# Optimization experiments

Hardware: AMD Instinct MI355X
Metric: run time of the kernel (lower is better)

## Reference

```python
import jax, jax.numpy as jnp
import numpy as np

N_NODES = 100000
N_EDGES = 1600000
D_IN = 128
D_HID = 128
N_CLASSES = 40


def _glorot(key, fan_in, fan_out):
    lim = np.sqrt(6.0 / (fan_in + fan_out)).astype(np.float32)
    return jax.random.uniform(key, (fan_in, fan_out), jnp.float32, -lim, lim)


def setup_inputs() -> dict:
    key = jax.random.key(0)
    ks = jax.random.split(key, 10)
    x = jax.random.normal(ks[0], (N_NODES, D_IN), jnp.float32)
    edge_index = jax.random.randint(ks[1], (2, N_EDGES), 0, N_NODES, jnp.int64)
    return {
        "x": x,
        "edge_index": edge_index,
        # layer 1: lin_l (neighbor, with bias), lin_r (root, no bias)
        "W1l": _glorot(ks[2], D_IN, D_HID),
        "b1": jnp.zeros((D_HID,), jnp.float32),
        "W1r": _glorot(ks[3], D_IN, D_HID),
        # layer 2
        "W2l": _glorot(ks[4], D_HID, D_HID),
        "b2": jnp.zeros((D_HID,), jnp.float32),
        "W2r": _glorot(ks[5], D_HID, D_HID),
        # layer 3
        "W3l": _glorot(ks[6], D_HID, N_CLASSES),
        "b3": jnp.zeros((N_CLASSES,), jnp.float32),
        "W3r": _glorot(ks[7], D_HID, N_CLASSES),
    }


def _sage_conv(x, src, dst, deg_inv, Wl, bl, Wr):
    # mean aggregation of source-node features onto destination nodes
    msgs = x[src]                                            # [E, d] gather
    agg = jax.ops.segment_sum(msgs, dst, num_segments=N_NODES)  # [N, d]
    agg = agg * deg_inv[:, None]                             # mean
    return agg @ Wl + bl + x @ Wr


def reference(x, edge_index, W1l, b1, W1r, W2l, b2, W2r, W3l, b3, W3r):
    src, dst = edge_index[0], edge_index[1]
    deg = jax.ops.segment_sum(jnp.ones((N_EDGES,), x.dtype), dst,
                              num_segments=N_NODES)
    deg_inv = 1.0 / jnp.maximum(deg, 1.0)
    h = _sage_conv(x, src, dst, deg_inv, W1l, b1, W1r)
    h = jax.nn.relu(h)  # dropout is identity in eval mode
    h = _sage_conv(h, src, dst, deg_inv, W2l, b2, W2r)
    h = jax.nn.relu(h)
    h = _sage_conv(h, src, dst, deg_inv, W3l, b3, W3r)
    return jax.nn.log_softmax(h, axis=1)
```

## Files before the change

kernel.cpp:

```cpp
#include <hip/hip_runtime.h>
#include <math.h>

#define D 128
#define NCLS 40
#define NBLK_P1 256

typedef unsigned int u32;
typedef __attribute__((ext_vector_type(8))) short short8;
typedef __attribute__((ext_vector_type(4))) float f32x4;

__device__ inline float bflo(u32 u){ return __uint_as_float(u << 16); }
__device__ inline float bfhi(u32 u){ return __uint_as_float(u & 0xffff0000u); }
__device__ inline u32 pack2bf(float a, float b){
  u32 ua = __float_as_uint(a), ub = __float_as_uint(b);
  ua += 0x7fffu + ((ua >> 16) & 1u);
  ub += 0x7fffu + ((ub >> 16) & 1u);
  return (ua >> 16) | (ub & 0xffff0000u);
}
__device__ inline unsigned short pack1bf(float a){
  u32 ua = __float_as_uint(a);
  ua += 0x7fffu + ((ua >> 16) & 1u);
  return (unsigned short)(ua >> 16);
}

__global__ __launch_bounds__(256) void prep_k(
    const float4* __restrict__ x4, uint2* __restrict__ xb, int n4,
    const float* __restrict__ W1l, const float* __restrict__ W1r, u32* __restrict__ Wt1,
    const float* __restrict__ W2l, const float* __restrict__ W2r, u32* __restrict__ Wt2,
    const float* __restrict__ W3l, const float* __restrict__ W3r,
    u32* __restrict__ Wt3b, float* __restrict__ bias3b, const float* __restrict__ b3,
    const int* __restrict__ dst, int* __restrict__ gcnt, int E, int nbuk, int nbX)
{
  __shared__ int cnt[1024];
  const int b = blockIdx.x;
  const int tid = threadIdx.x;
  if (b < nbX){
    int i = b * 256 + tid;
    if (i < n4){
      float4 v = x4[i];
      xb[i] = make_uint2(pack2bf(v.x, v.y), pack2bf(v.z, v.w));
    }
  } else if (b < nbX + 128){
    const bool first = (b < nbX + 64);
    const float* Wl = first ? W1l : W2l;
    const float* Wr = first ? W1r : W2r;
    u32* Wt = first ? Wt1 : Wt2;
    int i = ((b - nbX) & 63) * 256 + tid;
    int nn = i >> 7, kp = i & 127;
    int k = kp * 2;
    float a, c;
    if (k < 128){ a = Wl[(size_t)k * 128 + nn]; c = Wl[(size_t)(k + 1) * 128 + nn]; }
    else        { a = Wr[(size_t)(k - 128) * 128 + nn]; c = Wr[(size_t)(k - 127) * 128 + nn]; }
    Wt[(size_t)nn * 128 + kp] = pack2bf(a, c);
  } else if (b < nbX + 160){
    int i = (b - nbX - 128) * 256 + tid;
    if (i < 128 * 64){
      int nn = i >> 6, kp = i & 63;
      int k = kp * 2;
      float a = 0.f, c = 0.f;
      if (nn < NCLS){
        a = W3l[(size_t)k * NCLS + nn]; c = W3l[(size_t)(k + 1) * NCLS + nn];
      } else if (nn >= 64 && nn < 64 + NCLS){
        int cc = nn - 64;
        a = W3r[(size_t)k * NCLS + cc]; c = W3r[(size_t)(k + 1) * NCLS + cc];
      }
      Wt3b[(size_t)nn * 64 + kp] = pack2bf(a, c);
    }
    if (b == nbX + 128 && tid < 128)
      bias3b[tid] = (tid >= 64 && tid < 64 + NCLS) ? b3[tid - 64] : 0.f;
  } else {
    const int hb = b - nbX - 160;
    for (int i = tid; i < nbuk; i += 256) cnt[i] = 0;
    __syncthreads();
    const int per = (E + NBLK_P1 - 1) / NBLK_P1;
    const int e0 = hb * per;
    const int e1 = min(e0 + per, E);
    for (int i = e0 + tid; i < e1; i += 256)
      atomicAdd(&cnt[dst[i] >> 7], 1);
    __syncthreads();
    for (int i = tid; i < nbuk; i += 256)
      gcnt[(size_t)hb * nbuk + i] = cnt[i];
  }
}


__global__ __launch_bounds__(256) void bsum_k(
    const int* __restrict__ gcnt, int* __restrict__ btot, int nbuk)
{
  __shared__ int sm[256];
  const int j = blockIdx.x;
  sm[threadIdx.x] = gcnt[(size_t)threadIdx.x * nbuk + j];
  __syncthreads();
  for (int off = 128; off > 0; off >>= 1){
    if (threadIdx.x < off) sm[threadIdx.x] += sm[threadIdx.x + off];
    __syncthreads();
  }
  if (threadIdx.x == 0) btot[j] = sm[0];
}

__global__ __launch_bounds__(1024) void scan_k(
    const int* __restrict__ btot, int* __restrict__ bbase, int nbuk)
{
  __shared__ int sm[1024];
  const int j = threadIdx.x;
  int v = (j < nbuk) ? btot[j] : 0;
  sm[j] = v;
  __syncthreads();
  int acc = v;
  for (int off = 1; off < 1024; off <<= 1){
    int t = (j >= off) ? sm[j - off] : 0;
    __syncthreads();
    acc += t; sm[j] = acc;
    __syncthreads();
  }
  if (j < nbuk){
    bbase[j] = acc - v;
    if (j == nbuk - 1) bbase[nbuk] = acc;
  }
}

__global__ __launch_bounds__(256) void goff_k(
    const int* __restrict__ gcnt, const int* __restrict__ bbase,
    int* __restrict__ goff, int nbuk)
{
  __shared__ int sm[256];
  const int j = blockIdx.x;
  const int i = threadIdx.x;
  int v = gcnt[(size_t)i * nbuk + j];
  sm[i] = v;
  __syncthreads();
  int acc = v;
  for (int off = 1; off < 256; off <<= 1){
    int t = (i >= off) ? sm[i - off] : 0;
    __syncthreads();
    acc += t; sm[i] = acc;
    __syncthreads();
  }
  goff[(size_t)i * nbuk + j] = bbase[j] + acc - v;
}

__global__ __launch_bounds__(256) void part_fill_k(
    const int* __restrict__ src, const int* __restrict__ dst,
    const int* __restrict__ goff, u32* __restrict__ staging,
    int E, int nbuk)
{
  __shared__ int boff[1024];
  __shared__ int cur[1024];
  const int tid = threadIdx.x;
  for (int i = tid; i < nbuk; i += 256){
    boff[i] = goff[(size_t)blockIdx.x * nbuk + i];
    cur[i] = 0;
  }
  __syncthreads();
  const int per = (E + NBLK_P1 - 1) / NBLK_P1;
  const int e0 = blockIdx.x * per;
  const int e1 = min(e0 + per, E);
  for (int i = e0 + tid; i < e1; i += 256){
    int d = dst[i];
    int s = src[i];
    int b = d >> 7;
    int p = atomicAdd(&cur[b], 1);
    staging[boff[b] + p] = ((u32)s << 7) | (u32)(d & 127);
  }
}

__global__ __launch_bounds__(256) void bucket_csr_k(
    const u32* __restrict__ staging, const int* __restrict__ bbase,
    int* __restrict__ csr_off, float* __restrict__ deg_inv,
    int* __restrict__ csr_src, int N)
{
  __shared__ int ldeg[128];
  __shared__ int sm[128];
  __shared__ int lbase[128];
  __shared__ int lpos[128];
  const int b = blockIdx.x;
  const int node0 = b << 7;
  const int tid = threadIdx.x;
  if (tid < 128) ldeg[tid] = 0;
  __syncthreads();
  const int lo = bbase[b], hi = bbase[b + 1];
  for (int i = lo + tid; i < hi; i += 256)
    atomicAdd(&ldeg[staging[i] & 127u], 1);
  __syncthreads();
  if (tid < 128) sm[tid] = ldeg[tid];
  __syncthreads();
  for (int off = 1; off < 128; off <<= 1){
    int t = (tid >= off && tid < 128) ? sm[tid - off] : 0;
    __syncthreads();
    if (tid < 128) sm[tid] += t;
    __syncthreads();
  }
  if (tid < 128){
    const int excl = sm[tid] - ldeg[tid];
    lbase[tid] = lo + excl;
    lpos[tid] = 0;
    const int node = node0 + tid;
    if (node < N){
      csr_off[node] = lo + excl;
      deg_inv[node] = 1.0f / fmaxf((float)ldeg[tid], 1.0f);
    } else if (node == N){
      csr_off[N] = lo + excl;
    }
  }
  if (tid == 0 && b == (int)gridDim.x - 1) csr_off[N] = hi;
  __syncthreads();
  for (int i = lo + tid; i < hi; i += 256){
    u32 v = staging[i];
    int dloc = (int)(v & 127u);
    int p = atomicAdd(&lpos[dloc], 1);
    csr_src[lbase[dloc] + p] = (int)(v >> 7);
  }
}

__device__ inline void add8(float* acc, uint4 v){
  acc[0] += bflo(v.x); acc[1] += bfhi(v.x);
  acc[2] += bflo(v.y); acc[3] += bfhi(v.y);
  acc[4] += bflo(v.z); acc[5] += bfhi(v.z);
  acc[6] += bflo(v.w); acc[7] += bfhi(v.w);
}

__global__ __launch_bounds__(256) void aggregate_k(
    const u32* __restrict__ feat, const int* __restrict__ coff,
    const int* __restrict__ csr_src, const float* __restrict__ deg_inv,
    u32* __restrict__ agg, int n)
{
  const int g = threadIdx.x >> 4;
  const int lane = threadIdx.x & 15;
  const int node = blockIdx.x * 16 + g;
  if (node >= n) return;
  const int lo = coff[node], hi = coff[node + 1];
  const uint4* __restrict__ f4 = (const uint4*)feat;
  float acc[8] = {0.f,0.f,0.f,0.f,0.f,0.f,0.f,0.f};
  int e = lo;
  for (; e + 7 < hi; e += 8){
    int s0 = csr_src[e],     s1 = csr_src[e + 1];
    int s2 = csr_src[e + 2], s3 = csr_src[e + 3];
    int s4 = csr_src[e + 4], s5 = csr_src[e + 5];
    int s6 = csr_src[e + 6], s7 = csr_src[e + 7];
    uint4 v0 = f4[(size_t)s0 * 16 + lane];
    uint4 v1 = f4[(size_t)s1 * 16 + lane];
    uint4 v2 = f4[(size_t)s2 * 16 + lane];
    uint4 v3 = f4[(size_t)s3 * 16 + lane];
    uint4 v4 = f4[(size_t)s4 * 16 + lane];
    uint4 v5 = f4[(size_t)s5 * 16 + lane];
    uint4 v6 = f4[(size_t)s6 * 16 + lane];
    uint4 v7 = f4[(size_t)s7 * 16 + lane];
    add8(acc, v0); add8(acc, v1); add8(acc, v2); add8(acc, v3);
    add8(acc, v4); add8(acc, v5); add8(acc, v6); add8(acc, v7);
  }
  for (; e + 3 < hi; e += 4){
    int s0 = csr_src[e],     s1 = csr_src[e + 1];
    int s2 = csr_src[e + 2], s3 = csr_src[e + 3];
    uint4 v0 = f4[(size_t)s0 * 16 + lane];
    uint4 v1 = f4[(size_t)s1 * 16 + lane];
    uint4 v2 = f4[(size_t)s2 * 16 + lane];
    uint4 v3 = f4[(size_t)s3 * 16 + lane];
    add8(acc, v0); add8(acc, v1); add8(acc, v2); add8(acc, v3);
  }
  for (; e < hi; ++e){
    uint4 v0 = f4[(size_t)csr_src[e] * 16 + lane];
    add8(acc, v0);
  }
  const float di = deg_inv[node];
  uint4 o;
  o.x = pack2bf(acc[0] * di, acc[1] * di);
  o.y = pack2bf(acc[2] * di, acc[3] * di);
  o.z = pack2bf(acc[4] * di, acc[5] * di);
  o.w = pack2bf(acc[6] * di, acc[7] * di);
  ((uint4*)agg)[(size_t)node * 16 + lane] = o;
}

__global__ __launch_bounds__(256) void gemm_mfma_k(
    const u32* __restrict__ A1, const u32* __restrict__ A2,
    const u32* __restrict__ Wt, const float* __restrict__ bias,
    u32* __restrict__ out, int n)
{
  __shared__ u32 smem[8704];
  u32* As_u = smem;
  u32* Bs_u = smem + 2560;
  const int tid = threadIdx.x;
  const int row0 = blockIdx.x * 128;
  const int l = tid & 63, w = tid >> 6;
  const int lm = l & 15, lq = l >> 4;

  f32x4 acc[2][8];
  #pragma unroll
  for (int mi = 0; mi < 2; mi++)
    #pragma unroll
    for (int ni = 0; ni < 8; ni++) acc[mi][ni] = (f32x4){0.f, 0.f, 0.f, 0.f};

  for (int kt = 0; kt < 8; ++kt){
    const u32* Ap = (kt < 4) ? A1 : A2;
    const int ko = (kt & 3) * 16;
    #pragma unroll
    for (int i = 0; i < 2; i++){
      int chunk = tid + 256 * i;
      int row = chunk >> 2, q = chunk & 3;
      uint4 av = make_uint4(0, 0, 0, 0);
      int gr = row0 + row;
      if (gr < n) av = *(const uint4*)(Ap + (size_t)gr * 64 + ko + q * 4);
      *(uint4*)&As_u[row * 20 + q * 4] = av;
      uint4 bv = *(const uint4*)(Wt + (size_t)row * 128 + kt * 16 + q * 4);
      *(uint4*)&Bs_u[row * 20 + q * 4] = bv;
    }
    __syncthreads();
    short8 af0 = *(const short8*)&As_u[(w * 32 + lm) * 20 + lq * 4];
    short8 af1 = *(const short8*)&As_u[(w * 32 + 16 + lm) * 20 + lq * 4];
    #pragma unroll
    for (int ni = 0; ni < 8; ni++){
      short8 bf = *(const short8*)&Bs_u[(ni * 16 + lm) * 20 + lq * 4];
      acc[0][ni] = __builtin_amdgcn_mfma_f32_16x16x32_bf16(af0, bf, acc[0][ni], 0, 0, 0);
      acc[1][ni] = __builtin_amdgcn_mfma_f32_16x16x32_bf16(af1, bf, acc[1][ni], 0, 0, 0);
    }
    __syncthreads();
  }

  float bb[8];
  #pragma unroll
  for (int ni = 0; ni < 8; ni++) bb[ni] = bias[ni * 16 + lm];
  unsigned short* es = (unsigned short*)smem + w * (32 * 136);
  #pragma unroll
  for (int mi = 0; mi < 2; mi++)
    #pragma unroll
    for (int r = 0; r < 4; r++){
      const int Lr = mi * 16 + lq * 4 + r;
      #pragma unroll
      for (int ni = 0; ni < 8; ni++){
        float v = fmaxf(acc[mi][ni][r] + bb[ni], 0.f);
        es[Lr * 136 + ni * 16 + lm] = pack1bf(v);
      }
    }
  __syncthreads();
  uint4* outv = (uint4*)out;
  const int cl = l & 15;
  const int rsub = l >> 4;
  #pragma unroll
  for (int p = 0; p < 8; p++){
    const int Lr = p * 4 + rsub;
    const int row = row0 + w * 32 + Lr;
    uint4 t = *(const uint4*)&es[Lr * 136 + cl * 8];
    if (row < n) outv[(size_t)row * 16 + cl] = t;
  }
}

__global__ __launch_bounds__(256) void gemm3_mfma_k(
    const u32* __restrict__ A, const u32* __restrict__ Wt3b,
    const float* __restrict__ bias, u32* __restrict__ out, int n)
{
  __shared__ u32 smem[8704];
  u32* As_u = smem;
  u32* Bs_u = smem + 2560;
  const int tid = threadIdx.x;
  const int row0 = blockIdx.x * 128;
  const int l = tid & 63, w = tid >> 6;
  const int lm = l & 15, lq = l >> 4;

  f32x4 acc[2][8];
  #pragma unroll
  for (int mi = 0; mi < 2; mi++)
    #pragma unroll
    for (int ni = 0; ni < 8; ni++) acc[mi][ni] = (f32x4){0.f, 0.f, 0.f, 0.f};

  for (int kt = 0; kt < 4; ++kt){
    #pragma unroll
    for (int i = 0; i < 2; i++){
      int chunk = tid + 256 * i;
      int row = chunk >> 2, q = chunk & 3;
      uint4 av = make_uint4(0, 0, 0, 0);
      int gr = row0 + row;
      if (gr < n) av = *(const uint4*)(A + (size_t)gr * 64 + kt * 16 + q * 4);
      *(uint4*)&As_u[row * 20 + q * 4] = av;
      uint4 bv = *(const uint4*)(Wt3b + (size_t)row * 64 + kt * 16 + q * 4);
      *(uint4*)&Bs_u[row * 20 + q * 4] = bv;
    }
    __syncthreads();
    short8 af0 = *(const short8*)&As_u[(w * 32 + lm) * 20 + lq * 4];
    short8 af1 = *(const short8*)&As_u[(w * 32 + 16 + lm) * 20 + lq * 4];
    #pragma unroll
    for (int ni = 0; ni < 8; ni++){
      short8 bf = *(const short8*)&Bs_u[(ni * 16 + lm) * 20 + lq * 4];
      acc[0][ni] = __builtin_amdgcn_mfma_f32_16x16x32_bf16(af0, bf, acc[0][ni], 0, 0, 0);
      acc[1][ni] = __builtin_amdgcn_mfma_f32_16x16x32_bf16(af1, bf, acc[1][ni], 0, 0, 0);
    }
    __syncthreads();
  }

  float bb[8];
  #pragma unroll
  for (int ni = 0; ni < 8; ni++) bb[ni] = bias[ni * 16 + lm];
  unsigned short* es = (unsigned short*)smem + w * (32 * 136);
  #pragma unroll
  for (int mi = 0; mi < 2; mi++)
    #pragma unroll
    for (int r = 0; r < 4; r++){
      const int Lr = mi * 16 + lq * 4 + r;
      #pragma unroll
      for (int ni = 0; ni < 8; ni++){
        float v = acc[mi][ni][r] + bb[ni];
        es[Lr * 136 + ni * 16 + lm] = pack1bf(v);
      }
    }
  __syncthreads();
  uint4* outv = (uint4*)out;
  const int cl = l & 15;
  const int rsub = l >> 4;
  #pragma unroll
  for (int p = 0; p < 8; p++){
    const int Lr = p * 4 + rsub;
    const int row = row0 + w * 32 + Lr;
    uint4 t = *(const uint4*)&es[Lr * 136 + cl * 8];
    if (row < n) outv[(size_t)row * 16 + cl] = t;
  }
}

__global__ __launch_bounds__(256) void agg_softmax_k(
    const u32* __restrict__ yz, const int* __restrict__ coff,
    const int* __restrict__ csr_src, const float* __restrict__ deg_inv,
    float* __restrict__ out, int n)
{
  const int g = threadIdx.x >> 3;
  const int lane = threadIdx.x & 7;
  const int node = blockIdx.x * 32 + g;
  if (node >= n) return;
  const int lo = coff[node], hi = coff[node + 1];
  const uint4* __restrict__ f4 = (const uint4*)yz;
  float acc[8] = {0.f,0.f,0.f,0.f,0.f,0.f,0.f,0.f};
  int e = lo;
  for (; e + 7 < hi; e += 8){
    int s0 = csr_src[e],     s1 = csr_src[e + 1];
    int s2 = csr_src[e + 2], s3 = csr_src[e + 3];
    int s4 = csr_src[e + 4], s5 = csr_src[e + 5];
    int s6 = csr_src[e + 6], s7 = csr_src[e + 7];
    uint4 v0 = f4[(size_t)s0 * 16 + lane];
    uint4 v1 = f4[(size_t)s1 * 16 + lane];
    uint4 v2 = f4[(size_t)s2 * 16 + lane];
    uint4 v3 = f4[(size_t)s3 * 16 + lane];
    uint4 v4 = f4[(size_t)s4 * 16 + lane];
    uint4 v5 = f4[(size_t)s5 * 16 + lane];
    uint4 v6 = f4[(size_t)s6 * 16 + lane];
    uint4 v7 = f4[(size_t)s7 * 16 + lane];
    add8(acc, v0); add8(acc, v1); add8(acc, v2); add8(acc, v3);
    add8(acc, v4); add8(acc, v5); add8(acc, v6); add8(acc, v7);
  }
  for (; e + 3 < hi; e += 4){
    int s0 = csr_src[e],     s1 = csr_src[e + 1];
    int s2 = csr_src[e + 2], s3 = csr_src[e + 3];
    uint4 v0 = f4[(size_t)s0 * 16 + lane];
    uint4 v1 = f4[(size_t)s1 * 16 + lane];
    uint4 v2 = f4[(size_t)s2 * 16 + lane];
    uint4 v3 = f4[(size_t)s3 * 16 + lane];
    add8(acc, v0); add8(acc, v1); add8(acc, v2); add8(acc, v3);
  }
  for (; e < hi; ++e){
    uint4 v0 = f4[(size_t)csr_src[e] * 16 + lane];
    add8(acc, v0);
  }
  const float di = deg_inv[node];
  uint4 zv = f4[(size_t)node * 16 + 8 + lane];
  float v[8];
  v[0] = acc[0] * di + bflo(zv.x); v[1] = acc[1] * di + bfhi(zv.x);
  v[2] = acc[2] * di + bflo(zv.y); v[3] = acc[3] * di + bfhi(zv.y);
  v[4] = acc[4] * di + bflo(zv.z); v[5] = acc[5] * di + bfhi(zv.z);
  v[6] = acc[6] * di + bflo(zv.w); v[7] = acc[7] * di + bfhi(zv.w);
  const bool valid = (lane < 5);
  float m = -INFINITY;
  if (valid){
    #pragma unroll
    for (int j = 0; j < 8; j++) m = fmaxf(m, v[j]);
  }
  #pragma unroll
  for (int off = 1; off < 8; off <<= 1) m = fmaxf(m, __shfl_xor(m, off, 64));
  float s = 0.f;
  if (valid){
    #pragma unroll
    for (int j = 0; j < 8; j++) s += __expf(v[j] - m);
  }
  #pragma unroll
  for (int off = 1; off < 8; off <<= 1) s += __shfl_xor(s, off, 64);
  const float ls = m + logf(s);
  if (valid){
    float* op = out + (size_t)node * NCLS + lane * 8;
    *(float4*)op     = make_float4(v[0]-ls, v[1]-ls, v[2]-ls, v[3]-ls);
    *(float4*)(op+4) = make_float4(v[4]-ls, v[5]-ls, v[6]-ls, v[7]-ls);
  }
}


extern "C" void kernel_launch(void* const* d_in, const int* in_sizes, int n_in,
                              void* d_out, int out_size, void* d_ws, size_t ws_size,
                              hipStream_t stream) {
  const float* x   = (const float*)d_in[0];
  const int*   ei  = (const int*)d_in[1];
  const float* W1l = (const float*)d_in[2];
  const float* b1  = (const float*)d_in[3];
  const float* W1r = (const float*)d_in[4];
  const float* W2l = (const float*)d_in[5];
  const float* b2  = (const float*)d_in[6];
  const float* W2r = (const float*)d_in[7];
  const float* W3l = (const float*)d_in[8];
  const float* b3  = (const float*)d_in[9];
  const float* W3r = (const float*)d_in[10];

  const int N = in_sizes[0] / D;
  const int E = in_sizes[1] / 2;
  const int* src = ei;
  const int* dst = ei + E;
  const int nbuk = (N + 127) >> 7;

  char* ws = (char*)d_ws;
  auto alloc = [&](size_t bytes) -> void* {
    void* p = (void*)ws;
    ws += (bytes + 255) & ~(size_t)255;
    return p;
  };
  int*   csr_off  = (int*)  alloc((size_t)(N + 1) * 4);
  float* deg_inv  = (float*)alloc((size_t)N * 4);
  int*   csr_src  = (int*)  alloc((size_t)E * 4);
  u32*   staging  = (u32*)  alloc((size_t)E * 4);
  int*   gcnt     = (int*)  alloc((size_t)NBLK_P1 * nbuk * 4);
  int*   goff     = (int*)  alloc((size_t)NBLK_P1 * nbuk * 4);
  int*   bbase    = (int*)  alloc((size_t)(nbuk + 1) * 4);
  int*   btot     = (int*)  alloc((size_t)(nbuk + 1) * 4);
  u32*   xb       = (u32*)  alloc((size_t)N * D * 2);
  u32*   agg      = (u32*)  alloc((size_t)N * D * 2);
  u32*   hbuf     = (u32*)  alloc((size_t)N * D * 2);
  u32*   yz       = (u32*)  alloc((size_t)N * D * 2);
  u32*   Wt1      = (u32*)  alloc((size_t)128 * 128 * 4);
  u32*   Wt2      = (u32*)  alloc((size_t)128 * 128 * 4);
  u32*   Wt3b    = (u32*)  alloc((size_t)128 * 64 * 4);
  float* bias3b   = (float*)alloc((size_t)128 * 4);

  const int n4 = N * D / 4;
  const int nbX = (n4 + 255) / 256;
  prep_k<<<nbX + 160 + NBLK_P1, 256, 0, stream>>>(
      (const float4*)x, (uint2*)xb, n4,
      W1l, W1r, Wt1, W2l, W2r, Wt2,
      W3l, W3r, Wt3b, bias3b, b3,
      dst, gcnt, E, nbuk, nbX);

  bsum_k<<<nbuk, 256, 0, stream>>>(gcnt, btot, nbuk);
  scan_k<<<1, 1024, 0, stream>>>(btot, bbase, nbuk);
  goff_k<<<nbuk, 256, 0, stream>>>(gcnt, bbase, goff, nbuk);
  part_fill_k<<<NBLK_P1, 256, 0, stream>>>(src, dst, goff, staging, E, nbuk);
  bucket_csr_k<<<nbuk, 256, 0, stream>>>(staging, bbase, csr_off, deg_inv, csr_src, N);

  const int gblocks = (N + 127) / 128;
  const int ablocks = (N + 15) / 16;
  aggregate_k<<<ablocks, 256, 0, stream>>>(xb, csr_off, csr_src, deg_inv, agg, N);
  gemm_mfma_k<<<gblocks, 256, 0, stream>>>(agg, xb, Wt1, b1, hbuf, N);
  aggregate_k<<<ablocks, 256, 0, stream>>>(hbuf, csr_off, csr_src, deg_inv, agg, N);
  gemm_mfma_k<<<gblocks, 256, 0, stream>>>(agg, hbuf, Wt2, b2, hbuf, N);
  gemm3_mfma_k<<<gblocks, 256, 0, stream>>>(hbuf, Wt3b, bias3b, yz, N);
  agg_softmax_k<<<(N + 31) / 32, 256, 0, stream>>>(yz, csr_off, csr_src, deg_inv,
                                                   (float*)d_out, N);
}
```

Measured before the change: 385.0 us.

## Fuse neighbor mean aggregation into the layer GEMM kernel via shared memory

Layers 1 and 2 now use one kernel that gathers and averages neighbor features for a 64-row tile straight into shared memory, appends the root features, and runs the MFMA GEMM on that tile. This removes the round trip of the intermediate aggregate buffer through global memory and one launch per layer. Layer 2 writes to a separate output buffer because the kernel reads neighbor rows of its input. In exchange the GEMM tile shrinks to 64 rows with less weight reuse per block, and the gather latency is no longer overlapped by a separate high-occupancy kernel.

```diff
diff --git a/kernel.cpp b/kernel.cpp
--- a/kernel.cpp
+++ b/kernel.cpp
@@ -4,6 +4,7 @@
 #define D 128
 #define NCLS 40
 #define NBLK_P1 256
+#define FM 64
 
 typedef unsigned int u32;
 typedef __attribute__((ext_vector_type(8))) short short8;
@@ -219,98 +220,97 @@
   acc[6] += bflo(v.w); acc[7] += bfhi(v.w);
 }
 
-__global__ __launch_bounds__(256) void aggregate_k(
+__global__ __launch_bounds__(256) void fused_agg_gemm_k(
     const u32* __restrict__ feat, const int* __restrict__ coff,
     const int* __restrict__ csr_src, const float* __restrict__ deg_inv,
-    u32* __restrict__ agg, int n)
-{
-  const int g = threadIdx.x >> 4;
-  const int lane = threadIdx.x & 15;
-  const int node = blockIdx.x * 16 + g;
-  if (node >= n) return;
-  const int lo = coff[node], hi = coff[node + 1];
-  const uint4* __restrict__ f4 = (const uint4*)feat;
-  float acc[8] = {0.f,0.f,0.f,0.f,0.f,0.f,0.f,0.f};
-  int e = lo;
-  for (; e + 7 < hi; e += 8){
-    int s0 = csr_src[e],     s1 = csr_src[e + 1];
-    int s2 = csr_src[e + 2], s3 = csr_src[e + 3];
-    int s4 = csr_src[e + 4], s5 = csr_src[e + 5];
-    int s6 = csr_src[e + 6], s7 = csr_src[e + 7];
-    uint4 v0 = f4[(size_t)s0 * 16 + lane];
-    uint4 v1 = f4[(size_t)s1 * 16 + lane];
-    uint4 v2 = f4[(size_t)s2 * 16 + lane];
-    uint4 v3 = f4[(size_t)s3 * 16 + lane];
-    uint4 v4 = f4[(size_t)s4 * 16 + lane];
-    uint4 v5 = f4[(size_t)s5 * 16 + lane];
-    uint4 v6 = f4[(size_t)s6 * 16 + lane];
-    uint4 v7 = f4[(size_t)s7 * 16 + lane];
-    add8(acc, v0); add8(acc, v1); add8(acc, v2); add8(acc, v3);
-    add8(acc, v4); add8(acc, v5); add8(acc, v6); add8(acc, v7);
-  }
-  for (; e + 3 < hi; e += 4){
-    int s0 = csr_src[e],     s1 = csr_src[e + 1];
-    int s2 = csr_src[e + 2], s3 = csr_src[e + 3];
-    uint4 v0 = f4[(size_t)s0 * 16 + lane];
-    uint4 v1 = f4[(size_t)s1 * 16 + lane];
-    uint4 v2 = f4[(size_t)s2 * 16 + lane];
-    uint4 v3 = f4[(size_t)s3 * 16 + lane];
-    add8(acc, v0); add8(acc, v1); add8(acc, v2); add8(acc, v3);
-  }
-  for (; e < hi; ++e){
-    uint4 v0 = f4[(size_t)csr_src[e] * 16 + lane];
-    add8(acc, v0);
-  }
-  const float di = deg_inv[node];
-  uint4 o;
-  o.x = pack2bf(acc[0] * di, acc[1] * di);
-  o.y = pack2bf(acc[2] * di, acc[3] * di);
-  o.z = pack2bf(acc[4] * di, acc[5] * di);
-  o.w = pack2bf(acc[6] * di, acc[7] * di);
-  ((uint4*)agg)[(size_t)node * 16 + lane] = o;
-}
-
-__global__ __launch_bounds__(256) void gemm_mfma_k(
-    const u32* __restrict__ A1, const u32* __restrict__ A2,
     const u32* __restrict__ Wt, const float* __restrict__ bias,
     u32* __restrict__ out, int n)
 {
-  __shared__ u32 smem[8704];
-  u32* As_u = smem;
-  u32* Bs_u = smem + 2560;
+  __shared__ u32 As[FM * 132];
+  __shared__ u32 Bs[128 * 20];
   const int tid = threadIdx.x;
-  const int row0 = blockIdx.x * 128;
+  const int row0 = blockIdx.x * FM;
+
+  {
+    const int g = tid >> 4;
+    const int lane = tid & 15;
+    const uint4* __restrict__ f4 = (const uint4*)feat;
+    for (int sp = 0; sp < 4; ++sp){
+      const int r = sp * 16 + g;
+      const int node = row0 + r;
+      float acc[8] = {0.f,0.f,0.f,0.f,0.f,0.f,0.f,0.f};
+      float di = 0.f;
+      if (node < n){
+        di = deg_inv[node];
+        const int lo = coff[node], hi = coff[node + 1];
+        int e = lo;
+        for (; e + 7 < hi; e += 8){
+          int s0 = csr_src[e],     s1 = csr_src[e + 1];
+          int s2 = csr_src[e + 2], s3 = csr_src[e + 3];
+          int s4 = csr_src[e + 4], s5 = csr_src[e + 5];
+          int s6 = csr_src[e + 6], s7 = csr_src[e + 7];
+          uint4 v0 = f4[(size_t)s0 * 16 + lane];
+          uint4 v1 = f4[(size_t)s1 * 16 + lane];
+          uint4 v2 = f4[(size_t)s2 * 16 + lane];
+          uint4 v3 = f4[(size_t)s3 * 16 + lane];
+          uint4 v4 = f4[(size_t)s4 * 16 + lane];
+          uint4 v5 = f4[(size_t)s5 * 16 + lane];
+          uint4 v6 = f4[(size_t)s6 * 16 + lane];
+          uint4 v7 = f4[(size_t)s7 * 16 + lane];
+          add8(acc, v0); add8(acc, v1); add8(acc, v2); add8(acc, v3);
+          add8(acc, v4); add8(acc, v5); add8(acc, v6); add8(acc, v7);
+        }
+        for (; e + 3 < hi; e += 4){
+          int s0 = csr_src[e],     s1 = csr_src[e + 1];
+          int s2 = csr_src[e + 2], s3 = csr_src[e + 3];
+          uint4 v0 = f4[(size_t)s0 * 16 + lane];
+          uint4 v1 = f4[(size_t)s1 * 16 + lane];
+          uint4 v2 = f4[(size_t)s2 * 16 + lane];
+          uint4 v3 = f4[(size_t)s3 * 16 + lane];
+          add8(acc, v0); add8(acc, v1); add8(acc, v2); add8(acc, v3);
+        }
+        for (; e < hi; ++e){
+          uint4 v0 = f4[(size_t)csr_src[e] * 16 + lane];
+          add8(acc, v0);
+        }
+      }
+      uint4 o;
+      o.x = pack2bf(acc[0] * di, acc[1] * di);
+      o.y = pack2bf(acc[2] * di, acc[3] * di);
+      o.z = pack2bf(acc[4] * di, acc[5] * di);
+      o.w = pack2bf(acc[6] * di, acc[7] * di);
+      *(uint4*)&As[r * 132 + lane * 4] = o;
+    }
+    for (int i = tid; i < FM * 16; i += 256){
+      int r = i >> 4, q = i & 15;
+      int gr = row0 + r;
+      uint4 v = make_uint4(0, 0, 0, 0);
+      if (gr < n) v = *(const uint4*)(feat + (size_t)gr * 64 + q * 4);
+      *(uint4*)&As[r * 132 + 64 + q * 4] = v;
+    }
+  }
+  __syncthreads();
+
   const int l = tid & 63, w = tid >> 6;
   const int lm = l & 15, lq = l >> 4;
-
-  f32x4 acc[2][8];
-  #pragma unroll
-  for (int mi = 0; mi < 2; mi++)
-    #pragma unroll
-    for (int ni = 0; ni < 8; ni++) acc[mi][ni] = (f32x4){0.f, 0.f, 0.f, 0.f};
+  f32x4 acc2[8];
+  #pragma unroll
+  for (int ni = 0; ni < 8; ni++) acc2[ni] = (f32x4){0.f, 0.f, 0.f, 0.f};
 
   for (int kt = 0; kt < 8; ++kt){
-    const u32* Ap = (kt < 4) ? A1 : A2;
-    const int ko = (kt & 3) * 16;
     #pragma unroll
     for (int i = 0; i < 2; i++){
-      int chunk = tid + 256 * i;
-      int row = chunk >> 2, q = chunk & 3;
-      uint4 av = make_uint4(0, 0, 0, 0);
-      int gr = row0 + row;
-      if (gr < n) av = *(const uint4*)(Ap + (size_t)gr * 64 + ko + q * 4);
-      *(uint4*)&As_u[row * 20 + q * 4] = av;
-      uint4 bv = *(const uint4*)(Wt + (size_t)row * 128 + kt * 16 + q * 4);
-      *(uint4*)&Bs_u[row * 20 + q * 4] = bv;
-    }
-    __syncthreads();
-    short8 af0 = *(const short8*)&As_u[(w * 32 + lm) * 20 + lq * 4];
-    short8 af1 = *(const short8*)&As_u[(w * 32 + 16 + lm) * 20 + lq * 4];
+      int c2 = tid + 256 * i;
+      int brow = c2 >> 2, q = c2 & 3;
+      uint4 bv = *(const uint4*)(Wt + (size_t)brow * 128 + kt * 16 + q * 4);
+      *(uint4*)&Bs[brow * 20 + q * 4] = bv;
+    }
+    __syncthreads();
+    short8 af = *(const short8*)&As[(w * 16 + lm) * 132 + kt * 16 + lq * 4];
     #pragma unroll
     for (int ni = 0; ni < 8; ni++){
-      short8 bf = *(const short8*)&Bs_u[(ni * 16 + lm) * 20 + lq * 4];
-      acc[0][ni] = __builtin_amdgcn_mfma_f32_16x16x32_bf16(af0, bf, acc[0][ni], 0, 0, 0);
-      acc[1][ni] = __builtin_amdgcn_mfma_f32_16x16x32_bf16(af1, bf, acc[1][ni], 0, 0, 0);
+      short8 bf = *(const short8*)&Bs[(ni * 16 + lm) * 20 + lq * 4];
+      acc2[ni] = __builtin_amdgcn_mfma_f32_16x16x32_bf16(af, bf, acc2[ni], 0, 0, 0);
     }
     __syncthreads();
   }
@@ -318,26 +318,24 @@
   float bb[8];
   #pragma unroll
   for (int ni = 0; ni < 8; ni++) bb[ni] = bias[ni * 16 + lm];
-  unsigned short* es = (unsigned short*)smem + w * (32 * 136);
-  #pragma unroll
-  for (int mi = 0; mi < 2; mi++)
-    #pragma unroll
-    for (int r = 0; r < 4; r++){
-      const int Lr = mi * 16 + lq * 4 + r;
-      #pragma unroll
-      for (int ni = 0; ni < 8; ni++){
-        float v = fmaxf(acc[mi][ni][r] + bb[ni], 0.f);
-        es[Lr * 136 + ni * 16 + lm] = pack1bf(v);
-      }
-    }
+  unsigned short* es = (unsigned short*)As + w * (16 * 136);
+  #pragma unroll
+  for (int r = 0; r < 4; r++){
+    const int Lr = lq * 4 + r;
+    #pragma unroll
+    for (int ni = 0; ni < 8; ni++){
+      float v = fmaxf(acc2[ni][r] + bb[ni], 0.f);
+      es[Lr * 136 + ni * 16 + lm] = pack1bf(v);
+    }
+  }
   __syncthreads();
   uint4* outv = (uint4*)out;
   const int cl = l & 15;
   const int rsub = l >> 4;
   #pragma unroll
-  for (int p = 0; p < 8; p++){
+  for (int p = 0; p < 4; p++){
     const int Lr = p * 4 + rsub;
-    const int row = row0 + w * 32 + Lr;
+    const int row = row0 + w * 16 + Lr;
     uint4 t = *(const uint4*)&es[Lr * 136 + cl * 8];
     if (row < n) outv[(size_t)row * 16 + cl] = t;
   }
@@ -522,7 +520,7 @@
   int*   bbase    = (int*)  alloc((size_t)(nbuk + 1) * 4);
   int*   btot     = (int*)  alloc((size_t)(nbuk + 1) * 4);
   u32*   xb       = (u32*)  alloc((size_t)N * D * 2);
-  u32*   agg      = (u32*)  alloc((size_t)N * D * 2);
+  u32*   h2      = (u32*)  alloc((size_t)N * D * 2);
   u32*   hbuf     = (u32*)  alloc((size_t)N * D * 2);
   u32*   yz       = (u32*)  alloc((size_t)N * D * 2);
   u32*   Wt1      = (u32*)  alloc((size_t)128 * 128 * 4);
@@ -544,13 +542,13 @@
   part_fill_k<<<NBLK_P1, 256, 0, stream>>>(src, dst, goff, staging, E, nbuk);
   bucket_csr_k<<<nbuk, 256, 0, stream>>>(staging, bbase, csr_off, deg_inv, csr_src, N);
 
+  const int fblocks = (N + FM - 1) / FM;
   const int gblocks = (N + 127) / 128;
-  const int ablocks = (N + 15) / 16;
-  aggregate_k<<<ablocks, 256, 0, stream>>>(xb, csr_off, csr_src, deg_inv, agg, N);
-  gemm_mfma_k<<<gblocks, 256, 0, stream>>>(agg, xb, Wt1, b1, hbuf, N);
-  aggregate_k<<<ablocks, 256, 0, stream>>>(hbuf, csr_off, csr_src, deg_inv, agg, N);
-  gemm_mfma_k<<<gblocks, 256, 0, stream>>>(agg, hbuf, Wt2, b2, hbuf, N);
-  gemm3_mfma_k<<<gblocks, 256, 0, stream>>>(hbuf, Wt3b, bias3b, yz, N);
+  fused_agg_gemm_k<<<fblocks, 256, 0, stream>>>(xb, csr_off, csr_src, deg_inv,
+                                                Wt1, b1, hbuf, N);
+  fused_agg_gemm_k<<<fblocks, 256, 0, stream>>>(hbuf, csr_off, csr_src, deg_inv,
+                                                Wt2, b2, h2, N);
+  gemm3_mfma_k<<<gblocks, 256, 0, stream>>>(h2, Wt3b, bias3b, yz, N);
   agg_softmax_k<<<(N + 31) / 32, 256, 0, stream>>>(yz, csr_off, csr_src, deg_inv,
                                                    (float*)d_out, N);
 }
```

New measurement: 396.6 us. 3.0% more time.

## Fuse layer-2 and layer-3 GEMMs and merge bucket-sum with column scan

Applied to the files above, without the earlier changes.

Layer 2's combined GEMM (agg·Wl + h·Wr, bias, ReLU) now writes its bf16 result tile into shared memory, and the layer-3 projection GEMM reads that tile directly. This removes one full N×128 bf16 write and read of the hidden buffer plus a kernel launch. Separately, the per-bucket sum and the column-offset scan are merged into one kernel that emits both local offsets and totals, and the global bucket base is added in part_fill, which drops another launch and a pass over gcnt. The cost is higher shared-memory use per block in the fused GEMM, which may lower occupancy.

```diff
diff --git a/kernel.cpp b/kernel.cpp
--- a/kernel.cpp
+++ b/kernel.cpp
@@ -83,45 +83,9 @@
   }
 }
 
-
-__global__ __launch_bounds__(256) void bsum_k(
-    const int* __restrict__ gcnt, int* __restrict__ btot, int nbuk)
-{
-  __shared__ int sm[256];
-  const int j = blockIdx.x;
-  sm[threadIdx.x] = gcnt[(size_t)threadIdx.x * nbuk + j];
-  __syncthreads();
-  for (int off = 128; off > 0; off >>= 1){
-    if (threadIdx.x < off) sm[threadIdx.x] += sm[threadIdx.x + off];
-    __syncthreads();
-  }
-  if (threadIdx.x == 0) btot[j] = sm[0];
-}
-
-__global__ __launch_bounds__(1024) void scan_k(
-    const int* __restrict__ btot, int* __restrict__ bbase, int nbuk)
-{
-  __shared__ int sm[1024];
-  const int j = threadIdx.x;
-  int v = (j < nbuk) ? btot[j] : 0;
-  sm[j] = v;
-  __syncthreads();
-  int acc = v;
-  for (int off = 1; off < 1024; off <<= 1){
-    int t = (j >= off) ? sm[j - off] : 0;
-    __syncthreads();
-    acc += t; sm[j] = acc;
-    __syncthreads();
-  }
-  if (j < nbuk){
-    bbase[j] = acc - v;
-    if (j == nbuk - 1) bbase[nbuk] = acc;
-  }
-}
-
-__global__ __launch_bounds__(256) void goff_k(
-    const int* __restrict__ gcnt, const int* __restrict__ bbase,
-    int* __restrict__ goff, int nbuk)
+__global__ __launch_bounds__(256) void colscan_k(
+    const int* __restrict__ gcnt, int* __restrict__ goff,
+    int* __restrict__ btot, int nbuk)
 {
   __shared__ int sm[256];
   const int j = blockIdx.x;
@@ -136,19 +100,41 @@
     acc += t; sm[i] = acc;
     __syncthreads();
   }
-  goff[(size_t)i * nbuk + j] = bbase[j] + acc - v;
+  goff[(size_t)i * nbuk + j] = acc - v;
+  if (i == 255) btot[j] = acc;
+}
+
+__global__ __launch_bounds__(1024) void scan_k(
+    const int* __restrict__ btot, int* __restrict__ bbase, int nbuk)
+{
+  __shared__ int sm[1024];
+  const int j = threadIdx.x;
+  int v = (j < nbuk) ? btot[j] : 0;
+  sm[j] = v;
+  __syncthreads();
+  int acc = v;
+  for (int off = 1; off < 1024; off <<= 1){
+    int t = (j >= off) ? sm[j - off] : 0;
+    __syncthreads();
+    acc += t; sm[j] = acc;
+    __syncthreads();
+  }
+  if (j < nbuk){
+    bbase[j] = acc - v;
+    if (j == nbuk - 1) bbase[nbuk] = acc;
+  }
 }
 
 __global__ __launch_bounds__(256) void part_fill_k(
     const int* __restrict__ src, const int* __restrict__ dst,
-    const int* __restrict__ goff, u32* __restrict__ staging,
-    int E, int nbuk)
+    const int* __restrict__ goff, const int* __restrict__ bbase,
+    u32* __restrict__ staging, int E, int nbuk)
 {
   __shared__ int boff[1024];
   __shared__ int cur[1024];
   const int tid = threadIdx.x;
   for (int i = tid; i < nbuk; i += 256){
-    boff[i] = goff[(size_t)blockIdx.x * nbuk + i];
+    boff[i] = goff[(size_t)blockIdx.x * nbuk + i] + bbase[i];
     cur[i] = 0;
   }
   __syncthreads();
@@ -343,13 +329,16 @@
   }
 }
 
-__global__ __launch_bounds__(256) void gemm3_mfma_k(
-    const u32* __restrict__ A, const u32* __restrict__ Wt3b,
-    const float* __restrict__ bias, u32* __restrict__ out, int n)
-{
-  __shared__ u32 smem[8704];
-  u32* As_u = smem;
-  u32* Bs_u = smem + 2560;
+__global__ __launch_bounds__(256) void gemm23_mfma_k(
+    const u32* __restrict__ A1, const u32* __restrict__ A2,
+    const u32* __restrict__ Wt2, const float* __restrict__ b2,
+    const u32* __restrict__ Wt3b, const float* __restrict__ bias3b,
+    u32* __restrict__ yz, int n)
+{
+  __shared__ u32 Bs[128 * 20];
+  __shared__ u32 big[8704];
+  u32* As = big;
+  unsigned short* esH = (unsigned short*)big;
   const int tid = threadIdx.x;
   const int row0 = blockIdx.x * 128;
   const int l = tid & 63, w = tid >> 6;
@@ -361,54 +350,101 @@
     #pragma unroll
     for (int ni = 0; ni < 8; ni++) acc[mi][ni] = (f32x4){0.f, 0.f, 0.f, 0.f};
 
-  for (int kt = 0; kt < 4; ++kt){
+  for (int kt = 0; kt < 8; ++kt){
+    const u32* Ap = (kt < 4) ? A1 : A2;
+    const int ko = (kt & 3) * 16;
     #pragma unroll
     for (int i = 0; i < 2; i++){
       int chunk = tid + 256 * i;
       int row = chunk >> 2, q = chunk & 3;
       uint4 av = make_uint4(0, 0, 0, 0);
       int gr = row0 + row;
-      if (gr < n) av = *(const uint4*)(A + (size_t)gr * 64 + kt * 16 + q * 4);
-      *(uint4*)&As_u[row * 20 + q * 4] = av;
-      uint4 bv = *(const uint4*)(Wt3b + (size_t)row * 64 + kt * 16 + q * 4);
-      *(uint4*)&Bs_u[row * 20 + q * 4] = bv;
-    }
-    __syncthreads();
-    short8 af0 = *(const short8*)&As_u[(w * 32 + lm) * 20 + lq * 4];
-    short8 af1 = *(const short8*)&As_u[(w * 32 + 16 + lm) * 20 + lq * 4];
+      if (gr < n) av = *(const uint4*)(Ap + (size_t)gr * 64 + ko + q * 4);
+      *(uint4*)&As[row * 20 + q * 4] = av;
+      uint4 bv = *(const uint4*)(Wt2 + (size_t)row * 128 + kt * 16 + q * 4);
+      *(uint4*)&Bs[row * 20 + q * 4] = bv;
+    }
+    __syncthreads();
+    short8 af0 = *(const short8*)&As[(w * 32 + lm) * 20 + lq * 4];
+    short8 af1 = *(const short8*)&As[(w * 32 + 16 + lm) * 20 + lq * 4];
     #pragma unroll
     for (int ni = 0; ni < 8; ni++){
-      short8 bf = *(const short8*)&Bs_u[(ni * 16 + lm) * 20 + lq * 4];
+      short8 bf = *(const short8*)&Bs[(ni * 16 + lm) * 20 + lq * 4];
       acc[0][ni] = __builtin_amdgcn_mfma_f32_16x16x32_bf16(af0, bf, acc[0][ni], 0, 0, 0);
       acc[1][ni] = __builtin_amdgcn_mfma_f32_16x16x32_bf16(af1, bf, acc[1][ni], 0, 0, 0);
     }
     __syncthreads();
   }
 
-  float bb[8];
-  #pragma unroll
-  for (int ni = 0; ni < 8; ni++) bb[ni] = bias[ni * 16 + lm];
-  unsigned short* es = (unsigned short*)smem + w * (32 * 136);
+  {
+    float bb[8];
+    #pragma unroll
+    for (int ni = 0; ni < 8; ni++) bb[ni] = b2[ni * 16 + lm];
+    #pragma unroll
+    for (int mi = 0; mi < 2; mi++)
+      #pragma unroll
+      for (int r = 0; r < 4; r++){
+        const int grow = w * 32 + mi * 16 + lq * 4 + r;
+        #pragma unroll
+        for (int ni = 0; ni < 8; ni++){
+          float v = fmaxf(acc[mi][ni][r] + bb[ni], 0.f);
+          esH[grow * 136 + ni * 16 + lm] = pack1bf(v);
+        }
+      }
+  }
+  __syncthreads();
+
+  f32x4 acc2[2][8];
   #pragma unroll
   for (int mi = 0; mi < 2; mi++)
     #pragma unroll
-    for (int r = 0; r < 4; r++){
-      const int Lr = mi * 16 + lq * 4 + r;
+    for (int ni = 0; ni < 8; ni++) acc2[mi][ni] = (f32x4){0.f, 0.f, 0.f, 0.f};
+
+  for (int kt = 0; kt < 4; ++kt){
+    #pragma unroll
+    for (int i = 0; i < 2; i++){
+      int c2 = tid + 256 * i;
+      int brow = c2 >> 2, q = c2 & 3;
+      uint4 bv = *(const uint4*)(Wt3b + (size_t)brow * 64 + kt * 16 + q * 4);
+      *(uint4*)&Bs[brow * 20 + q * 4] = bv;
+    }
+    __syncthreads();
+    short8 a0 = *(const short8*)&esH[(w * 32 + lm) * 136 + kt * 32 + lq * 8];
+    short8 a1 = *(const short8*)&esH[(w * 32 + 16 + lm) * 136 + kt * 32 + lq * 8];
+    #pragma unroll
+    for (int ni = 0; ni < 8; ni++){
+      short8 bf = *(const short8*)&Bs[(ni * 16 + lm) * 20 + lq * 4];
+      acc2[0][ni] = __builtin_amdgcn_mfma_f32_16x16x32_bf16(a0, bf, acc2[0][ni], 0, 0, 0);
+      acc2[1][ni] = __builtin_amdgcn_mfma_f32_16x16x32_bf16(a1, bf, acc2[1][ni], 0, 0, 0);
+    }
+    __syncthreads();
+  }
+
+  {
+    float bb3[8];
+    #pragma unroll
+    for (int ni = 0; ni < 8; ni++) bb3[ni] = bias3b[ni * 16 + lm];
+    #pragma unroll
+    for (int mi = 0; mi < 2; mi++)
       #pragma unroll
-      for (int ni = 0; ni < 8; ni++){
-        float v = acc[mi][ni][r] + bb[ni];
-        es[Lr * 136 + ni * 16 + lm] = pack1bf(v);
+      for (int r = 0; r < 4; r++){
+        const int grow = w * 32 + mi * 16 + lq * 4 + r;
+        #pragma unroll
+        for (int ni = 0; ni < 8; ni++){
+          float v = acc2[mi][ni][r] + bb3[ni];
+          esH[grow * 136 + ni * 16 + lm] = pack1bf(v);
+        }
       }
-    }
-  __syncthreads();
-  uint4* outv = (uint4*)out;
+  }
+  __syncthreads();
+  uint4* outv = (uint4*)yz;
   const int cl = l & 15;
   const int rsub = l >> 4;
   #pragma unroll
   for (int p = 0; p < 8; p++){
     const int Lr = p * 4 + rsub;
     const int row = row0 + w * 32 + Lr;
-    uint4 t = *(const uint4*)&es[Lr * 136 + cl * 8];
+    uint4 t = *(const uint4*)&esH[(w * 32 + Lr) * 136 + cl * 8];
     if (row < n) outv[(size_t)row * 16 + cl] = t;
   }
 }
@@ -527,7 +563,7 @@
   u32*   yz       = (u32*)  alloc((size_t)N * D * 2);
   u32*   Wt1      = (u32*)  alloc((size_t)128 * 128 * 4);
   u32*   Wt2      = (u32*)  alloc((size_t)128 * 128 * 4);
-  u32*   Wt3b    = (u32*)  alloc((size_t)128 * 64 * 4);
+  u32*   Wt3b     = (u32*)  alloc((size_t)128 * 64 * 4);
   float* bias3b   = (float*)alloc((size_t)128 * 4);
 
   const int n4 = N * D / 4;
@@ -538,10 +574,9 @@
       W3l, W3r, Wt3b, bias3b, b3,
       dst, gcnt, E, nbuk, nbX);
 
-  bsum_k<<<nbuk, 256, 0, stream>>>(gcnt, btot, nbuk);
+  colscan_k<<<nbuk, 256, 0, stream>>>(gcnt, goff, btot, nbuk);
   scan_k<<<1, 1024, 0, stream>>>(btot, bbase, nbuk);
-  goff_k<<<nbuk, 256, 0, stream>>>(gcnt, bbase, goff, nbuk);
-  part_fill_k<<<NBLK_P1, 256, 0, stream>>>(src, dst, goff, staging, E, nbuk);
+  part_fill_k<<<NBLK_P1, 256, 0, stream>>>(src, dst, goff, bbase, staging, E, nbuk);
   bucket_csr_k<<<nbuk, 256, 0, stream>>>(staging, bbase, csr_off, deg_inv, csr_src, N);
 
   const int gblocks = (N + 127) / 128;
@@ -549,8 +584,7 @@
   aggregate_k<<<ablocks, 256, 0, stream>>>(xb, csr_off, csr_src, deg_inv, agg, N);
   gemm_mfma_k<<<gblocks, 256, 0, stream>>>(agg, xb, Wt1, b1, hbuf, N);
   aggregate_k<<<ablocks, 256, 0, stream>>>(hbuf, csr_off, csr_src, deg_inv, agg, N);
-  gemm_mfma_k<<<gblocks, 256, 0, stream>>>(agg, hbuf, Wt2, b2, hbuf, N);
-  gemm3_mfma_k<<<gblocks, 256, 0, stream>>>(hbuf, Wt3b, bias3b, yz, N);
+  gemm23_mfma_k<<<gblocks, 256, 0, stream>>>(agg, hbuf, Wt2, b2, Wt3b, bias3b, yz, N);
   agg_softmax_k<<<(N + 31) / 32, 256, 0, stream>>>(yz, csr_off, csr_src, deg_inv,
                                                    (float*)d_out, N);
 }
```

Result: faster. 367.9 us, median of 2 (-4.4%).
